# Optimization experiments

Measured on AMD Instinct MI355X. Metric: run time of the kernel, lower is better.

## Reference

```python
import jax, jax.numpy as jnp
import numpy as np

MAXDISP = 48
NUM_GROUPS = 40
CONCAT_CH = 12
BN_EPS = 1e-5


def conv3d(x, w):
    # x: [B,C,D,H,W], w: [O,I,3,3,3], stride 1, pad 1
    return jax.lax.conv_general_dilated(
        x, w, window_strides=(1, 1, 1), padding=[(1, 1), (1, 1), (1, 1)],
        dimension_numbers=('NCDHW', 'OIDHW', 'NCDHW'))


def bn_relu(x, gamma, beta, mean, var):
    # inference-style BatchNorm3d followed by ReLU
    inv = gamma * jax.lax.rsqrt(var + BN_EPS)
    sh = (1, -1, 1, 1, 1)
    return jax.nn.relu(x * inv.reshape(sh) + (beta - mean * inv).reshape(sh))


def build_volume(lg, rg, lc, rc):
    # Fused gwc + concat volume: for disparity d, valid region is columns [d:].
    # Columns [:d] are zero (matches the torch new_zeros + sliced writes).
    B, Cg, H, W = lg.shape
    cpg = Cg // NUM_GROUPS
    slices = []
    for d in range(MAXDISP):  # fixed structural loop over disparities
        if d == 0:
            l, r, lcc, rcc = lg, rg, lc, rc
        else:
            l = lg[:, :, :, d:]
            r = rg[:, :, :, :W - d]
            lcc = lc[:, :, :, d:]
            rcc = rc[:, :, :, :W - d]
        corr = (l * r).reshape(B, NUM_GROUPS, cpg, H, W - d).mean(axis=2)
        s = jnp.concatenate([corr, lcc, rcc], axis=1)  # [B, G+2Cc, H, W-d]
        if d > 0:
            s = jnp.pad(s, ((0, 0), (0, 0), (0, 0), (d, 0)))
        slices.append(s)
    return jnp.stack(slices, axis=2)  # [B, G+2Cc, D, H, W]


def setup_inputs() -> dict:
    key = jax.random.key(0)
    ks = jax.random.split(key, 10)
    B, H, W = 4, 64, 128
    Cin = NUM_GROUPS + 2 * CONCAT_CH  # 64
    f32 = jnp.float32
    return {
        'left_gwc': jax.random.normal(ks[0], (B, 320, H, W), f32),
        'right_gwc': jax.random.normal(ks[1], (B, 320, H, W), f32),
        'left_concat': jax.random.normal(ks[2], (B, CONCAT_CH, H, W), f32),
        'right_concat': jax.random.normal(ks[3], (B, CONCAT_CH, H, W), f32),
        'w1': jax.random.normal(ks[4], (32, Cin, 3, 3, 3), f32) * 0.05,
        'g1': jnp.ones((32,), f32),
        'b1': jnp.zeros((32,), f32),
        'm1': jnp.zeros((32,), f32),
        'v1': jnp.ones((32,), f32),
        'w2': jax.random.normal(ks[5], (32, 32, 3, 3, 3), f32) * 0.05,
        'g2': jnp.ones((32,), f32),
        'b2': jnp.zeros((32,), f32),
        'm2': jnp.zeros((32,), f32),
        'v2': jnp.ones((32,), f32),
    }


def reference(left_gwc, right_gwc, left_concat, right_concat,
              w1, g1, b1, m1, v1, w2, g2, b2, m2, v2):
    vol = build_volume(left_gwc, right_gwc, left_concat, right_concat)
    x = bn_relu(conv3d(vol, w1), g1, b1, m1, v1)
    x = bn_relu(conv3d(x, w2), g2, b2, m2, v2)
    return x  # [B, 32, D, H, W]
```

## Files before the change

kernel.cpp:

```cpp
#include <hip/hip_runtime.h>
#include <cstdint>
#include <cstddef>

typedef unsigned short u16;
typedef __bf16 bf16x8 __attribute__((ext_vector_type(8)));
typedef float f32x4 __attribute__((ext_vector_type(4)));

#define MAXDISP 48
#define HH 64
#define WW 128

__device__ __forceinline__ float bf2f(unsigned int x) {
    union { unsigned int i; float f; } c; c.i = x << 16; return c.f;
}
__device__ __forceinline__ float bf2f_hi(unsigned int x) {
    union { unsigned int i; float f; } c; c.i = x & 0xffff0000u; return c.f;
}
__device__ __forceinline__ u16 f2bf(float f) {
    union { float f; unsigned int i; } c; c.f = f;
    unsigned int x = c.i;
    return (u16)((x + 0x7fffu + ((x >> 16) & 1u)) >> 16);
}

__global__ __launch_bounds__(256) void wfrag_kernel(
    const float* __restrict__ w, const float* __restrict__ gam,
    const float* __restrict__ bet, const float* __restrict__ mea,
    const float* __restrict__ var,
    u16* __restrict__ dst, float* __restrict__ bias, int CIN, int KC)
{
    int idx = blockIdx.x * 256 + threadIdx.x;
    int n = 9 * 2 * KC * 512;
    if (idx < n) {
        int j    = idx & 7;
        int lane = (idx >> 3) & 63;
        int t2   = idx >> 9;
        int kc   = t2 % KC;
        int t3   = t2 / KC;
        int nt   = t3 & 1;
        int tap  = t3 >> 1;
        int co   = nt * 16 + (lane & 15);
        int qq   = lane >> 4;
        int kw, c;
        if (CIN == 64) { kw = kc >> 1; c = (kc & 1) * 32 + qq * 8 + j; }
        else           { kw = kc;      c = qq * 8 + j; }
        int kd = tap / 3, kh = tap % 3;
        float inv = gam[co] * rsqrtf(var[co] + 1e-5f);
        dst[idx] = f2bf(w[((size_t)co * CIN + c) * 27 + kd * 9 + kh * 3 + kw] * inv);
    }
    if (blockIdx.x == 0 && threadIdx.x < 32) {
        int co = threadIdx.x;
        float inv = gam[co] * rsqrtf(var[co] + 1e-5f);
        bias[co] = bet[co] - mea[co] * inv;
    }
}

#define RS 334
__global__ __launch_bounds__(256) void vol_build_kernel(
    const float* __restrict__ lg, const float* __restrict__ rg,
    const float* __restrict__ lc, const float* __restrict__ rc,
    u16* __restrict__ vol, int b0)
{
    __shared__ u16 r_s[128 * RS];
    __shared__ u16 o_s[4 * 128 * 68];

    int bi  = blockIdx.x;
    int h   = bi & 63;
    int dh  = (bi >> 6) & 1;
    int bl  = bi >> 7;
    int b   = b0 + bl;
    int tid = threadIdx.x;
    int w    = tid & 127;
    int part = tid >> 7;

    for (int idx = tid; idx < 320 * 32; idx += 256) {
        int c = idx >> 5, w4 = (idx & 31) << 2;
        const float4 v = *(const float4*)(rg + (((size_t)b * 320 + c) * 64 + h) * 128 + w4);
        r_s[(w4 + 0) * RS + c] = f2bf(v.x);
        r_s[(w4 + 1) * RS + c] = f2bf(v.y);
        r_s[(w4 + 2) * RS + c] = f2bf(v.z);
        r_s[(w4 + 3) * RS + c] = f2bf(v.w);
    }
    for (int idx = tid; idx < 12 * 32; idx += 256) {
        int c = idx >> 5, w4 = (idx & 31) << 2;
        const float4 v = *(const float4*)(rc + (((size_t)b * 12 + c) * 64 + h) * 128 + w4);
        r_s[(w4 + 0) * RS + 320 + c] = f2bf(v.x);
        r_s[(w4 + 1) * RS + 320 + c] = f2bf(v.y);
        r_s[(w4 + 2) * RS + 320 + c] = f2bf(v.z);
        r_s[(w4 + 3) * RS + 320 + c] = f2bf(v.w);
    }
    u16 lcv[12];
    if (part == 0) {
#pragma unroll
        for (int k = 0; k < 12; k++)
            lcv[k] = f2bf(lc[(((size_t)b * 12 + k) * 64 + h) * 128 + w]);
    }
    __syncthreads();

    int d0 = dh * 24;
    for (int dc = 0; dc < 24; dc += 4) {
        for (int gb = 0; gb < 5; gb++) {
            int g0 = part * 20 + gb * 4;
            float lv[4][8];
#pragma unroll
            for (int gg = 0; gg < 4; gg++)
#pragma unroll
                for (int j = 0; j < 8; j++)
                    lv[gg][j] = lg[(((size_t)b * 320 + (g0 + gg) * 8 + j) * 64 + h) * 128 + w];
#pragma unroll
            for (int dl = 0; dl < 4; dl++) {
                int d = d0 + dc + dl;
                union { u16 us[4]; uint2 u2; } pk;
                pk.us[0] = pk.us[1] = pk.us[2] = pk.us[3] = 0;
                if (w >= d) {
#pragma unroll
                    for (int gg = 0; gg < 4; gg++) {
                        float s = 0.f;
                        int base = (w - d) * RS + (g0 + gg) * 8;
#pragma unroll
                        for (int jj = 0; jj < 4; jj++) {
                            unsigned int uu = *(const unsigned int*)&r_s[base + jj * 2];
                            s += lv[gg][jj * 2]     * bf2f(uu & 0xffffu);
                            s += lv[gg][jj * 2 + 1] * bf2f_hi(uu);
                        }
                        pk.us[gg] = f2bf(s * 0.125f);
                    }
                }
                *(uint2*)&o_s[(dl * 128 + w) * 68 + g0] = pk.u2;
            }
        }
#pragma unroll
        for (int dl = 0; dl < 4; dl++) {
            int d = d0 + dc + dl;
            union { u16 us[12]; uint2 u2[3]; } z;
            if (part == 0) {
#pragma unroll
                for (int k = 0; k < 12; k++) z.us[k] = (w >= d) ? lcv[k] : (u16)0;
                u16* dst = &o_s[(dl * 128 + w) * 68 + 40];
                *(uint2*)(dst + 0) = z.u2[0];
                *(uint2*)(dst + 4) = z.u2[1];
                *(uint2*)(dst + 8) = z.u2[2];
            } else {
                if (w >= d) {
                    int base = (w - d) * RS + 320;
#pragma unroll
                    for (int k = 0; k < 12; k++) z.us[k] = r_s[base + k];
                } else {
#pragma unroll
                    for (int k = 0; k < 12; k++) z.us[k] = 0;
                }
                u16* dst = &o_s[(dl * 128 + w) * 68 + 52];
                *(uint2*)(dst + 0) = z.u2[0];
                *(uint2*)(dst + 4) = z.u2[1];
                *(uint2*)(dst + 8) = z.u2[2];
            }
        }
        __syncthreads();
#pragma unroll
        for (int i = 0; i < 16; i++) {
            int idx = i * 256 + tid;
            int dl  = idx >> 10;
            int rem = idx & 1023;
            int ww  = rem >> 3, cg = rem & 7;
            const u16* sp = &o_s[(dl * 128 + ww) * 68 + cg * 8];
            uint2 lo = *(const uint2*)sp;
            uint2 hi = *(const uint2*)(sp + 4);
            uint4 ov = { lo.x, lo.y, hi.x, hi.y };
            int d = d0 + dc + dl;
            *(uint4*)(vol + ((((size_t)bl * 48 + d) * 64 + h) * 128 + ww) * 64 + cg * 8) = ov;
        }
        __syncthreads();
    }
}

__global__ __launch_bounds__(256) void conv1_mfma_kernel(
    const u16* __restrict__ vol, const u16* __restrict__ wf,
    const float* __restrict__ bias, u16* __restrict__ x1)
{
    __shared__ u16 a_s[1170 * 8];

    int bi = blockIdx.x;
    int h  = bi & 63;
    int t1 = bi >> 6;
    int d  = t1 % 48;
    int bl = t1 / 48;
    int tid  = threadIdx.x;
    int lane = tid & 63, wid = tid >> 6;
    int lm = lane & 15, q = lane >> 4;

    f32x4 acc[2][2];
#pragma unroll
    for (int i = 0; i < 2; i++)
#pragma unroll
        for (int j = 0; j < 2; j++) acc[i][j] = { 0.f, 0.f, 0.f, 0.f };

    for (int kd = 0; kd < 3; kd++) {
        int dd = d + kd - 1;
        if (dd < 0 || dd >= 48) continue;
        for (int kh = 0; kh < 3; kh++) {
            int hh = h + kh - 1;
            if (hh < 0 || hh >= 64) continue;
            int tap = kd * 3 + kh;

            __syncthreads();
            const u16* src = vol + (((size_t)bl * 48 + dd) * 64 + hh) * 8192;
#pragma unroll
            for (int i = 0; i < 4; i++) {
                int idx = i * 256 + tid;
                int wp = (idx >> 3) + 1, cg = idx & 7;
                uint4 v = *(const uint4*)(src + idx * 8);
                *(uint4*)&a_s[(wp * 9 + cg) * 8] = v;
            }
            if (tid < 16) {
                uint4 z = { 0, 0, 0, 0 };
                int wp = (tid >> 3) ? 129 : 0;
                *(uint4*)&a_s[(wp * 9 + (tid & 7)) * 8] = z;
            }
            __syncthreads();

            bf16x8 bfr[2][6];
#pragma unroll
            for (int nt = 0; nt < 2; nt++)
#pragma unroll
                for (int kc = 0; kc < 6; kc++)
                    bfr[nt][kc] = *(const bf16x8*)(wf + (((size_t)tap * 2 + nt) * 6 + kc) * 512 + lane * 8);

#pragma unroll
            for (int kc = 0; kc < 6; kc++) {
                int kw = kc >> 1;
                int cg = (kc & 1) * 4 + q;
#pragma unroll
                for (int mt = 0; mt < 2; mt++) {
                    int wp = (wid * 2 + mt) * 16 + lm + kw;
                    bf16x8 afr = *(const bf16x8*)&a_s[(wp * 9 + cg) * 8];
                    acc[mt][0] = __builtin_amdgcn_mfma_f32_16x16x32_bf16(afr, bfr[0][kc], acc[mt][0], 0, 0, 0);
                    acc[mt][1] = __builtin_amdgcn_mfma_f32_16x16x32_bf16(afr, bfr[1][kc], acc[mt][1], 0, 0, 0);
                }
            }
        }
    }

    u16* xb = x1 + (((size_t)bl * 48 + d) * 64 + h) * 4096;
#pragma unroll
    for (int mt = 0; mt < 2; mt++)
#pragma unroll
        for (int nt = 0; nt < 2; nt++) {
            int co = nt * 16 + lm;
            float bs = bias[co];
#pragma unroll
            for (int r = 0; r < 4; r++) {
                int w = (wid * 2 + mt) * 16 + q * 4 + r;
                xb[w * 32 + co] = f2bf(fmaxf(acc[mt][nt][r] + bs, 0.f));
            }
        }
}

__global__ __launch_bounds__(256) void conv2_mfma_kernel(
    const u16* __restrict__ x1, const u16* __restrict__ wf,
    const float* __restrict__ bias, float* __restrict__ out, int b0)
{
    __shared__ u16 a_s[650 * 8];

    int bi = blockIdx.x;
    int h  = bi & 63;
    int t1 = bi >> 6;
    int d  = t1 % 48;
    int bl = t1 / 48;
    int tid  = threadIdx.x;
    int lane = tid & 63, wid = tid >> 6;
    int lm = lane & 15, q = lane >> 4;

    f32x4 acc[2][2];
#pragma unroll
    for (int i = 0; i < 2; i++)
#pragma unroll
        for (int j = 0; j < 2; j++) acc[i][j] = { 0.f, 0.f, 0.f, 0.f };

    for (int kd = 0; kd < 3; kd++) {
        int dd = d + kd - 1;
        if (dd < 0 || dd >= 48) continue;
        for (int kh = 0; kh < 3; kh++) {
            int hh = h + kh - 1;
            if (hh < 0 || hh >= 64) continue;
            int tap = kd * 3 + kh;

            __syncthreads();
            const u16* src = x1 + (((size_t)bl * 48 + dd) * 64 + hh) * 4096;
#pragma unroll
            for (int i = 0; i < 2; i++) {
                int idx = i * 256 + tid;
                int wp = (idx >> 2) + 1, cg = idx & 3;
                uint4 v = *(const uint4*)(src + idx * 8);
                *(uint4*)&a_s[(wp * 5 + cg) * 8] = v;
            }
            if (tid < 8) {
                uint4 z = { 0, 0, 0, 0 };
                int wp = (tid >> 2) ? 129 : 0;
                *(uint4*)&a_s[(wp * 5 + (tid & 3)) * 8] = z;
            }
            __syncthreads();

            bf16x8 bfr[2][3];
#pragma unroll
            for (int nt = 0; nt < 2; nt++)
#pragma unroll
                for (int kc = 0; kc < 3; kc++)
                    bfr[nt][kc] = *(const bf16x8*)(wf + (((size_t)tap * 2 + nt) * 3 + kc) * 512 + lane * 8);

#pragma unroll
            for (int kc = 0; kc < 3; kc++) {
                int kw = kc;
#pragma unroll
                for (int mt = 0; mt < 2; mt++) {
                    int wp = (wid * 2 + mt) * 16 + lm + kw;
                    bf16x8 afr = *(const bf16x8*)&a_s[(wp * 5 + q) * 8];
                    acc[mt][0] = __builtin_amdgcn_mfma_f32_16x16x32_bf16(afr, bfr[0][kc], acc[mt][0], 0, 0, 0);
                    acc[mt][1] = __builtin_amdgcn_mfma_f32_16x16x32_bf16(afr, bfr[1][kc], acc[mt][1], 0, 0, 0);
                }
            }
        }
    }

#pragma unroll
    for (int mt = 0; mt < 2; mt++)
#pragma unroll
        for (int nt = 0; nt < 2; nt++) {
            int co = nt * 16 + lm;
            float bs = bias[co];
            float4 o;
            o.x = fmaxf(acc[mt][nt][0] + bs, 0.f);
            o.y = fmaxf(acc[mt][nt][1] + bs, 0.f);
            o.z = fmaxf(acc[mt][nt][2] + bs, 0.f);
            o.w = fmaxf(acc[mt][nt][3] + bs, 0.f);
            int wbase = (wid * 2 + mt) * 16 + q * 4;
            *(float4*)(out + ((((size_t)(b0 + bl) * 32 + co) * 48 + d) * 64 + h) * 128 + wbase) = o;
        }
}

extern "C" void kernel_launch(void* const* d_in, const int* in_sizes, int n_in,
                              void* d_out, int out_size, void* d_ws, size_t ws_size,
                              hipStream_t stream)
{
    const float* lg = (const float*)d_in[0];
    const float* rg = (const float*)d_in[1];
    const float* lc = (const float*)d_in[2];
    const float* rc = (const float*)d_in[3];
    const float* w1 = (const float*)d_in[4];
    const float* g1 = (const float*)d_in[5];
    const float* b1 = (const float*)d_in[6];
    const float* m1 = (const float*)d_in[7];
    const float* v1 = (const float*)d_in[8];
    const float* w2 = (const float*)d_in[9];
    const float* g2 = (const float*)d_in[10];
    const float* b2 = (const float*)d_in[11];
    const float* m2 = (const float*)d_in[12];
    const float* v2 = (const float*)d_in[13];
    (void)in_sizes; (void)n_in; (void)out_size; (void)ws_size;

    char* ws = (char*)d_ws;
    u16*   wf1   = (u16*)ws;
    u16*   wf2   = (u16*)(ws + 110592);
    float* bias1 = (float*)(ws + 165888);
    float* bias2 = (float*)(ws + 166016);
    u16*   x1    = (u16*)(ws + 166144);

    wfrag_kernel<<<216, 256, 0, stream>>>(w1, g1, b1, m1, v1, wf1, bias1, 64, 6);
    wfrag_kernel<<<108, 256, 0, stream>>>(w2, g2, b2, m2, v2, wf2, bias2, 32, 3);

    for (int r = 0; r < 2; r++) {
        u16* vol = (u16*)d_out + (size_t)r * 50331648;
        vol_build_kernel<<<256, 256, 0, stream>>>(lg, rg, lc, rc, vol, 2 * r);
        conv1_mfma_kernel<<<6144, 256, 0, stream>>>(vol, wf1, bias1, x1);
        conv2_mfma_kernel<<<6144, 256, 0, stream>>>(x1, wf2, bias2, (float*)d_out, 2 * r);
    }
}
```

Before: 802.5 us.

## Tile conv kernels over 2x2 output depth-height blocks to reuse input rows

Each conv block now computes a 2x2 tile of output (depth, height) rows. It loads the 4 overlapping input height rows per depth slice into shared memory once and reuses them across all four outputs, instead of reloading 9 input rows per output row. conv1 splits the 64 input channels into two 32-channel chunks to fit shared memory. The volume-build kernel is split into 4 depth quarters to double its grid. This raises accumulator register pressure (launch_bounds 256,3) and cuts the conv grids by four.

After: 979.1 us. 22.0% more time.

```diff
diff --git a/kernel.cpp b/kernel.cpp
--- a/kernel.cpp
+++ b/kernel.cpp
@@ -65,8 +65,8 @@
 
     int bi  = blockIdx.x;
     int h   = bi & 63;
-    int dh  = (bi >> 6) & 1;
-    int bl  = bi >> 7;
+    int dq  = (bi >> 6) & 3;
+    int bl  = bi >> 8;
     int b   = b0 + bl;
     int tid = threadIdx.x;
     int w    = tid & 127;
@@ -96,8 +96,8 @@
     }
     __syncthreads();
 
-    int d0 = dh * 24;
-    for (int dc = 0; dc < 24; dc += 4) {
+    int d0 = dq * 12;
+    for (int dc = 0; dc < 12; dc += 4) {
         for (int gb = 0; gb < 5; gb++) {
             int g0 = part * 20 + gb * 4;
             float lv[4][8];
@@ -172,168 +172,212 @@
     }
 }
 
-__global__ __launch_bounds__(256) void conv1_mfma_kernel(
+__global__ __launch_bounds__(256, 3) void conv1_mfma_kernel(
     const u16* __restrict__ vol, const u16* __restrict__ wf,
     const float* __restrict__ bias, u16* __restrict__ x1)
 {
-    __shared__ u16 a_s[1170 * 8];
+    __shared__ u16 a_s[4][5200];
 
     int bi = blockIdx.x;
-    int h  = bi & 63;
-    int t1 = bi >> 6;
-    int d  = t1 % 48;
-    int bl = t1 / 48;
+    int ht = bi & 31;
+    int dt = (bi >> 5) % 24;
+    int bl = bi / 768;
+    int h0 = ht * 2, d0 = dt * 2;
     int tid  = threadIdx.x;
     int lane = tid & 63, wid = tid >> 6;
     int lm = lane & 15, q = lane >> 4;
 
-    f32x4 acc[2][2];
-#pragma unroll
-    for (int i = 0; i < 2; i++)
-#pragma unroll
-        for (int j = 0; j < 2; j++) acc[i][j] = { 0.f, 0.f, 0.f, 0.f };
-
-    for (int kd = 0; kd < 3; kd++) {
-        int dd = d + kd - 1;
+    f32x4 acc[2][2][2][2];
+#pragma unroll
+    for (int a = 0; a < 2; a++)
+#pragma unroll
+        for (int o = 0; o < 2; o++)
+#pragma unroll
+            for (int m = 0; m < 2; m++)
+#pragma unroll
+                for (int n = 0; n < 2; n++) acc[a][o][m][n] = { 0.f, 0.f, 0.f, 0.f };
+
+#pragma unroll 1
+    for (int dr = 0; dr < 4; dr++) {
+        int dd = d0 - 1 + dr;
         if (dd < 0 || dd >= 48) continue;
-        for (int kh = 0; kh < 3; kh++) {
-            int hh = h + kh - 1;
-            if (hh < 0 || hh >= 64) continue;
-            int tap = kd * 3 + kh;
-
+        const u16* srcbase = vol + ((size_t)bl * 48 + dd) * 64 * 8192;
+        int od0v = (dr <= 2), od1v = (dr >= 1);
+
+#pragma unroll 1
+        for (int ch = 0; ch < 2; ch++) {
             __syncthreads();
-            const u16* src = vol + (((size_t)bl * 48 + dd) * 64 + hh) * 8192;
-#pragma unroll
-            for (int i = 0; i < 4; i++) {
+#pragma unroll
+            for (int i = 0; i < 8; i++) {
                 int idx = i * 256 + tid;
-                int wp = (idx >> 3) + 1, cg = idx & 7;
-                uint4 v = *(const uint4*)(src + idx * 8);
-                *(uint4*)&a_s[(wp * 9 + cg) * 8] = v;
-            }
-            if (tid < 16) {
+                int r = idx >> 9, rem = idx & 511;
+                int w = rem >> 2, cg = rem & 3;
+                int hh = h0 - 1 + r;
+                uint4 v = { 0, 0, 0, 0 };
+                if (hh >= 0 && hh < 64)
+                    v = *(const uint4*)(srcbase + (size_t)hh * 8192 + w * 64 + ch * 32 + cg * 8);
+                *(uint4*)&a_s[r][((w + 1) * 5 + cg) * 8] = v;
+            }
+            if (tid < 32) {
                 uint4 z = { 0, 0, 0, 0 };
-                int wp = (tid >> 3) ? 129 : 0;
-                *(uint4*)&a_s[(wp * 9 + (tid & 7)) * 8] = z;
+                int r = tid >> 3, side = (tid >> 2) & 1, cg = tid & 3;
+                *(uint4*)&a_s[r][((side ? 129 : 0) * 5 + cg) * 8] = z;
             }
             __syncthreads();
 
-            bf16x8 bfr[2][6];
-#pragma unroll
-            for (int nt = 0; nt < 2; nt++)
-#pragma unroll
-                for (int kc = 0; kc < 6; kc++)
-                    bfr[nt][kc] = *(const bf16x8*)(wf + (((size_t)tap * 2 + nt) * 6 + kc) * 512 + lane * 8);
-
-#pragma unroll
-            for (int kc = 0; kc < 6; kc++) {
-                int kw = kc >> 1;
-                int cg = (kc & 1) * 4 + q;
-#pragma unroll
-                for (int mt = 0; mt < 2; mt++) {
-                    int wp = (wid * 2 + mt) * 16 + lm + kw;
-                    bf16x8 afr = *(const bf16x8*)&a_s[(wp * 9 + cg) * 8];
-                    acc[mt][0] = __builtin_amdgcn_mfma_f32_16x16x32_bf16(afr, bfr[0][kc], acc[mt][0], 0, 0, 0);
-                    acc[mt][1] = __builtin_amdgcn_mfma_f32_16x16x32_bf16(afr, bfr[1][kc], acc[mt][1], 0, 0, 0);
-                }
-            }
-        }
-    }
-
-    u16* xb = x1 + (((size_t)bl * 48 + d) * 64 + h) * 4096;
-#pragma unroll
-    for (int mt = 0; mt < 2; mt++)
-#pragma unroll
-        for (int nt = 0; nt < 2; nt++) {
-            int co = nt * 16 + lm;
-            float bs = bias[co];
 #pragma unroll
             for (int r = 0; r < 4; r++) {
-                int w = (wid * 2 + mt) * 16 + q * 4 + r;
-                xb[w * 32 + co] = f2bf(fmaxf(acc[mt][nt][r] + bs, 0.f));
-            }
-        }
-}
-
-__global__ __launch_bounds__(256) void conv2_mfma_kernel(
+#pragma unroll
+                for (int kw = 0; kw < 3; kw++) {
+                    int kc = kw * 2 + ch;
+                    bf16x8 afr[2];
+#pragma unroll
+                    for (int mt = 0; mt < 2; mt++)
+                        afr[mt] = *(const bf16x8*)&a_s[r][((((wid * 2 + mt) * 16 + lm + kw) * 5) + q) * 8];
+#pragma unroll
+                    for (int od = 0; od < 2; od++) {
+                        if (od == 0 ? !od0v : !od1v) continue;
+                        int kd = dr - od;
+#pragma unroll
+                        for (int oh = 0; oh < 2; oh++) {
+                            if (oh == 0 ? (r > 2) : (r < 1)) continue;
+                            int kh = r - oh;
+                            int tap = kd * 3 + kh;
+                            const u16* wp0 = wf + ((size_t)(tap * 2) * 6 + kc) * 512 + lane * 8;
+                            bf16x8 b0 = *(const bf16x8*)wp0;
+                            bf16x8 b1 = *(const bf16x8*)(wp0 + 6 * 512);
+#pragma unroll
+                            for (int mt = 0; mt < 2; mt++) {
+                                acc[od][oh][mt][0] = __builtin_amdgcn_mfma_f32_16x16x32_bf16(afr[mt], b0, acc[od][oh][mt][0], 0, 0, 0);
+                                acc[od][oh][mt][1] = __builtin_amdgcn_mfma_f32_16x16x32_bf16(afr[mt], b1, acc[od][oh][mt][1], 0, 0, 0);
+                            }
+                        }
+                    }
+                }
+            }
+        }
+    }
+
+#pragma unroll
+    for (int od = 0; od < 2; od++)
+#pragma unroll
+        for (int oh = 0; oh < 2; oh++) {
+            u16* xb = x1 + (((size_t)bl * 48 + d0 + od) * 64 + h0 + oh) * 4096;
+#pragma unroll
+            for (int mt = 0; mt < 2; mt++)
+#pragma unroll
+                for (int nt = 0; nt < 2; nt++) {
+                    int co = nt * 16 + lm;
+                    float bs = bias[co];
+#pragma unroll
+                    for (int rr = 0; rr < 4; rr++) {
+                        int w = (wid * 2 + mt) * 16 + q * 4 + rr;
+                        xb[w * 32 + co] = f2bf(fmaxf(acc[od][oh][mt][nt][rr] + bs, 0.f));
+                    }
+                }
+        }
+}
+
+__global__ __launch_bounds__(256, 3) void conv2_mfma_kernel(
     const u16* __restrict__ x1, const u16* __restrict__ wf,
     const float* __restrict__ bias, float* __restrict__ out, int b0)
 {
-    __shared__ u16 a_s[650 * 8];
+    __shared__ u16 a_s[4][5200];
 
     int bi = blockIdx.x;
-    int h  = bi & 63;
-    int t1 = bi >> 6;
-    int d  = t1 % 48;
-    int bl = t1 / 48;
+    int ht = bi & 31;
+    int dt = (bi >> 5) % 24;
+    int bl = bi / 768;
+    int h0 = ht * 2, d0 = dt * 2;
     int tid  = threadIdx.x;
     int lane = tid & 63, wid = tid >> 6;
     int lm = lane & 15, q = lane >> 4;
 
-    f32x4 acc[2][2];
-#pragma unroll
-    for (int i = 0; i < 2; i++)
-#pragma unroll
-        for (int j = 0; j < 2; j++) acc[i][j] = { 0.f, 0.f, 0.f, 0.f };
-
-    for (int kd = 0; kd < 3; kd++) {
-        int dd = d + kd - 1;
+    f32x4 acc[2][2][2][2];
+#pragma unroll
+    for (int a = 0; a < 2; a++)
+#pragma unroll
+        for (int o = 0; o < 2; o++)
+#pragma unroll
+            for (int m = 0; m < 2; m++)
+#pragma unroll
+                for (int n = 0; n < 2; n++) acc[a][o][m][n] = { 0.f, 0.f, 0.f, 0.f };
+
+#pragma unroll 1
+    for (int dr = 0; dr < 4; dr++) {
+        int dd = d0 - 1 + dr;
         if (dd < 0 || dd >= 48) continue;
-        for (int kh = 0; kh < 3; kh++) {
-            int hh = h + kh - 1;
-            if (hh < 0 || hh >= 64) continue;
-            int tap = kd * 3 + kh;
-
-            __syncthreads();
-            const u16* src = x1 + (((size_t)bl * 48 + dd) * 64 + hh) * 4096;
-#pragma unroll
-            for (int i = 0; i < 2; i++) {
-                int idx = i * 256 + tid;
-                int wp = (idx >> 2) + 1, cg = idx & 3;
-                uint4 v = *(const uint4*)(src + idx * 8);
-                *(uint4*)&a_s[(wp * 5 + cg) * 8] = v;
-            }
-            if (tid < 8) {
-                uint4 z = { 0, 0, 0, 0 };
-                int wp = (tid >> 2) ? 129 : 0;
-                *(uint4*)&a_s[(wp * 5 + (tid & 3)) * 8] = z;
-            }
-            __syncthreads();
-
-            bf16x8 bfr[2][3];
-#pragma unroll
-            for (int nt = 0; nt < 2; nt++)
-#pragma unroll
-                for (int kc = 0; kc < 3; kc++)
-                    bfr[nt][kc] = *(const bf16x8*)(wf + (((size_t)tap * 2 + nt) * 3 + kc) * 512 + lane * 8);
-
-#pragma unroll
-            for (int kc = 0; kc < 3; kc++) {
-                int kw = kc;
-#pragma unroll
-                for (int mt = 0; mt < 2; mt++) {
-                    int wp = (wid * 2 + mt) * 16 + lm + kw;
-                    bf16x8 afr = *(const bf16x8*)&a_s[(wp * 5 + q) * 8];
-                    acc[mt][0] = __builtin_amdgcn_mfma_f32_16x16x32_bf16(afr, bfr[0][kc], acc[mt][0], 0, 0, 0);
-                    acc[mt][1] = __builtin_amdgcn_mfma_f32_16x16x32_bf16(afr, bfr[1][kc], acc[mt][1], 0, 0, 0);
-                }
-            }
-        }
-    }
-
-#pragma unroll
-    for (int mt = 0; mt < 2; mt++)
-#pragma unroll
-        for (int nt = 0; nt < 2; nt++) {
-            int co = nt * 16 + lm;
-            float bs = bias[co];
-            float4 o;
-            o.x = fmaxf(acc[mt][nt][0] + bs, 0.f);
-            o.y = fmaxf(acc[mt][nt][1] + bs, 0.f);
-            o.z = fmaxf(acc[mt][nt][2] + bs, 0.f);
-            o.w = fmaxf(acc[mt][nt][3] + bs, 0.f);
-            int wbase = (wid * 2 + mt) * 16 + q * 4;
-            *(float4*)(out + ((((size_t)(b0 + bl) * 32 + co) * 48 + d) * 64 + h) * 128 + wbase) = o;
-        }
+        const u16* srcbase = x1 + ((size_t)bl * 48 + dd) * 64 * 4096;
+        int od0v = (dr <= 2), od1v = (dr >= 1);
+
+        __syncthreads();
+#pragma unroll
+        for (int i = 0; i < 8; i++) {
+            int idx = i * 256 + tid;
+            int r = idx >> 9, rem = idx & 511;
+            int w = rem >> 2, cg = rem & 3;
+            int hh = h0 - 1 + r;
+            uint4 v = { 0, 0, 0, 0 };
+            if (hh >= 0 && hh < 64)
+                v = *(const uint4*)(srcbase + (size_t)hh * 4096 + w * 32 + cg * 8);
+            *(uint4*)&a_s[r][((w + 1) * 5 + cg) * 8] = v;
+        }
+        if (tid < 32) {
+            uint4 z = { 0, 0, 0, 0 };
+            int r = tid >> 3, side = (tid >> 2) & 1, cg = tid & 3;
+            *(uint4*)&a_s[r][((side ? 129 : 0) * 5 + cg) * 8] = z;
+        }
+        __syncthreads();
+
+#pragma unroll
+        for (int r = 0; r < 4; r++) {
+#pragma unroll
+            for (int kw = 0; kw < 3; kw++) {
+                bf16x8 afr[2];
+#pragma unroll
+                for (int mt = 0; mt < 2; mt++)
+                    afr[mt] = *(const bf16x8*)&a_s[r][((((wid * 2 + mt) * 16 + lm + kw) * 5) + q) * 8];
+#pragma unroll
+                for (int od = 0; od < 2; od++) {
+                    if (od == 0 ? !od0v : !od1v) continue;
+                    int kd = dr - od;
+#pragma unroll
+                    for (int oh = 0; oh < 2; oh++) {
+                        if (oh == 0 ? (r > 2) : (r < 1)) continue;
+                        int kh = r - oh;
+                        int tap = kd * 3 + kh;
+                        const u16* wp0 = wf + ((size_t)(tap * 2) * 3 + kw) * 512 + lane * 8;
+                        bf16x8 b0 = *(const bf16x8*)wp0;
+                        bf16x8 b1 = *(const bf16x8*)(wp0 + 3 * 512);
+#pragma unroll
+                        for (int mt = 0; mt < 2; mt++) {
+                            acc[od][oh][mt][0] = __builtin_amdgcn_mfma_f32_16x16x32_bf16(afr[mt], b0, acc[od][oh][mt][0], 0, 0, 0);
+                            acc[od][oh][mt][1] = __builtin_amdgcn_mfma_f32_16x16x32_bf16(afr[mt], b1, acc[od][oh][mt][1], 0, 0, 0);
+                        }
+                    }
+                }
+            }
+        }
+    }
+
+#pragma unroll
+    for (int od = 0; od < 2; od++)
+#pragma unroll
+        for (int oh = 0; oh < 2; oh++)
+#pragma unroll
+            for (int mt = 0; mt < 2; mt++)
+#pragma unroll
+                for (int nt = 0; nt < 2; nt++) {
+                    int co = nt * 16 + lm;
+                    float bs = bias[co];
+                    float4 o;
+                    o.x = fmaxf(acc[od][oh][mt][nt][0] + bs, 0.f);
+                    o.y = fmaxf(acc[od][oh][mt][nt][1] + bs, 0.f);
+                    o.z = fmaxf(acc[od][oh][mt][nt][2] + bs, 0.f);
+                    o.w = fmaxf(acc[od][oh][mt][nt][3] + bs, 0.f);
+                    int wbase = (wid * 2 + mt) * 16 + q * 4;
+                    *(float4*)(out + ((((size_t)(b0 + bl) * 32 + co) * 48 + d0 + od) * 64 + h0 + oh) * 128 + wbase) = o;
+                }
 }
 
 extern "C" void kernel_launch(void* const* d_in, const int* in_sizes, int n_in,
@@ -368,8 +412,8 @@
 
     for (int r = 0; r < 2; r++) {
         u16* vol = (u16*)d_out + (size_t)r * 50331648;
-        vol_build_kernel<<<256, 256, 0, stream>>>(lg, rg, lc, rc, vol, 2 * r);
-        conv1_mfma_kernel<<<6144, 256, 0, stream>>>(vol, wf1, bias1, x1);
-        conv2_mfma_kernel<<<6144, 256, 0, stream>>>(x1, wf2, bias2, (float*)d_out, 2 * r);
-    }
-}
+        vol_build_kernel<<<512, 256, 0, stream>>>(lg, rg, lc, rc, vol, 2 * r);
+        conv1_mfma_kernel<<<1536, 256, 0, stream>>>(vol, wf1, bias1, x1);
+        conv2_mfma_kernel<<<1536, 256, 0, stream>>>(x1, wf2, bias2, (float*)d_out, 2 * r);
+    }
+}
```

## Double-buffer conv input rows with register prefetch and split volume build finer

Applied to the files above, without the earlier changes.

The conv1 and conv2 kernels now list their valid taps up front and use double-buffered shared memory. Each loop iteration prefetches the next tap's input row into registers while the current tap's MFMAs run, which removes one barrier per tap and hides global load latency. Launch bounds now request minimum occupancy. The volume build splits disparities into quarters instead of halves, launching twice as many blocks for better CU coverage. In exchange, each volume block reloads and converts the full right-feature row, doubling that redundant work, and conv shared memory and register use go up.

New measurement: 1.546 ms. 92.6% more time.

```diff
diff --git a/kernel.cpp b/kernel.cpp
--- a/kernel.cpp
+++ b/kernel.cpp
@@ -65,8 +65,8 @@
 
     int bi  = blockIdx.x;
     int h   = bi & 63;
-    int dh  = (bi >> 6) & 1;
-    int bl  = bi >> 7;
+    int dq  = (bi >> 6) & 3;
+    int bl  = bi >> 8;
     int b   = b0 + bl;
     int tid = threadIdx.x;
     int w    = tid & 127;
@@ -96,8 +96,8 @@
     }
     __syncthreads();
 
-    int d0 = dh * 24;
-    for (int dc = 0; dc < 24; dc += 4) {
+    int d0 = dq * 12;
+    for (int dc = 0; dc < 12; dc += 4) {
         for (int gb = 0; gb < 5; gb++) {
             int g0 = part * 20 + gb * 4;
             float lv[4][8];
@@ -172,11 +172,11 @@
     }
 }
 
-__global__ __launch_bounds__(256) void conv1_mfma_kernel(
+__global__ __launch_bounds__(256, 3) void conv1_mfma_kernel(
     const u16* __restrict__ vol, const u16* __restrict__ wf,
     const float* __restrict__ bias, u16* __restrict__ x1)
 {
-    __shared__ u16 a_s[1170 * 8];
+    __shared__ u16 a_s[2][1170 * 8];
 
     int bi = blockIdx.x;
     int h  = bi & 63;
@@ -187,54 +187,74 @@
     int lane = tid & 63, wid = tid >> 6;
     int lm = lane & 15, q = lane >> 4;
 
-    f32x4 acc[2][2];
-#pragma unroll
-    for (int i = 0; i < 2; i++)
-#pragma unroll
-        for (int j = 0; j < 2; j++) acc[i][j] = { 0.f, 0.f, 0.f, 0.f };
-
+    if (tid < 32) {
+        uint4 z = { 0, 0, 0, 0 };
+        int bsel = tid >> 4, side = (tid >> 3) & 1, cg = tid & 7;
+        *(uint4*)&a_s[bsel][((side ? 129 : 0) * 9 + cg) * 8] = z;
+    }
+
+    int trow[9], ttap[9], ntap = 0;
     for (int kd = 0; kd < 3; kd++) {
         int dd = d + kd - 1;
         if (dd < 0 || dd >= 48) continue;
         for (int kh = 0; kh < 3; kh++) {
             int hh = h + kh - 1;
             if (hh < 0 || hh >= 64) continue;
-            int tap = kd * 3 + kh;
-
-            __syncthreads();
-            const u16* src = vol + (((size_t)bl * 48 + dd) * 64 + hh) * 8192;
-#pragma unroll
-            for (int i = 0; i < 4; i++) {
-                int idx = i * 256 + tid;
-                int wp = (idx >> 3) + 1, cg = idx & 7;
-                uint4 v = *(const uint4*)(src + idx * 8);
-                *(uint4*)&a_s[(wp * 9 + cg) * 8] = v;
-            }
-            if (tid < 16) {
-                uint4 z = { 0, 0, 0, 0 };
-                int wp = (tid >> 3) ? 129 : 0;
-                *(uint4*)&a_s[(wp * 9 + (tid & 7)) * 8] = z;
-            }
-            __syncthreads();
-
-            bf16x8 bfr[2][6];
-#pragma unroll
-            for (int nt = 0; nt < 2; nt++)
-#pragma unroll
-                for (int kc = 0; kc < 6; kc++)
-                    bfr[nt][kc] = *(const bf16x8*)(wf + (((size_t)tap * 2 + nt) * 6 + kc) * 512 + lane * 8);
-
-#pragma unroll
-            for (int kc = 0; kc < 6; kc++) {
-                int kw = kc >> 1;
-                int cg = (kc & 1) * 4 + q;
-#pragma unroll
-                for (int mt = 0; mt < 2; mt++) {
-                    int wp = (wid * 2 + mt) * 16 + lm + kw;
-                    bf16x8 afr = *(const bf16x8*)&a_s[(wp * 9 + cg) * 8];
-                    acc[mt][0] = __builtin_amdgcn_mfma_f32_16x16x32_bf16(afr, bfr[0][kc], acc[mt][0], 0, 0, 0);
-                    acc[mt][1] = __builtin_amdgcn_mfma_f32_16x16x32_bf16(afr, bfr[1][kc], acc[mt][1], 0, 0, 0);
-                }
+            trow[ntap] = dd * 64 + hh;
+            ttap[ntap] = kd * 3 + kh;
+            ntap++;
+        }
+    }
+    const u16* vbase = vol + (size_t)bl * 48 * 64 * 8192;
+
+    f32x4 acc[2][2];
+#pragma unroll
+    for (int i = 0; i < 2; i++)
+#pragma unroll
+        for (int j = 0; j < 2; j++) acc[i][j] = { 0.f, 0.f, 0.f, 0.f };
+
+    uint4 pf[4];
+    {
+        const u16* src = vbase + (size_t)trow[0] * 8192;
+#pragma unroll
+        for (int i = 0; i < 4; i++) pf[i] = *(const uint4*)(src + (i * 256 + tid) * 8);
+    }
+
+#pragma unroll 1
+    for (int t = 0; t < ntap; t++) {
+        u16* buf = a_s[t & 1];
+#pragma unroll
+        for (int i = 0; i < 4; i++) {
+            int idx = i * 256 + tid;
+            int wp = (idx >> 3) + 1, cg = idx & 7;
+            *(uint4*)&buf[(wp * 9 + cg) * 8] = pf[i];
+        }
+        __syncthreads();
+
+        int tap = ttap[t];
+        bf16x8 bfr[2][6];
+#pragma unroll
+        for (int nt = 0; nt < 2; nt++)
+#pragma unroll
+            for (int kc = 0; kc < 6; kc++)
+                bfr[nt][kc] = *(const bf16x8*)(wf + (((size_t)tap * 2 + nt) * 6 + kc) * 512 + lane * 8);
+
+        if (t + 1 < ntap) {
+            const u16* src = vbase + (size_t)trow[t + 1] * 8192;
+#pragma unroll
+            for (int i = 0; i < 4; i++) pf[i] = *(const uint4*)(src + (i * 256 + tid) * 8);
+        }
+
+#pragma unroll
+        for (int kc = 0; kc < 6; kc++) {
+            int kw = kc >> 1;
+            int cg = (kc & 1) * 4 + q;
+#pragma unroll
+            for (int mt = 0; mt < 2; mt++) {
+                int wp = (wid * 2 + mt) * 16 + lm + kw;
+                bf16x8 afr = *(const bf16x8*)&buf[(wp * 9 + cg) * 8];
+                acc[mt][0] = __builtin_amdgcn_mfma_f32_16x16x32_bf16(afr, bfr[0][kc], acc[mt][0], 0, 0, 0);
+                acc[mt][1] = __builtin_amdgcn_mfma_f32_16x16x32_bf16(afr, bfr[1][kc], acc[mt][1], 0, 0, 0);
             }
         }
     }
@@ -254,11 +274,11 @@
         }
 }
 
-__global__ __launch_bounds__(256) void conv2_mfma_kernel(
+__global__ __launch_bounds__(256, 4) void conv2_mfma_kernel(
     const u16* __restrict__ x1, const u16* __restrict__ wf,
     const float* __restrict__ bias, float* __restrict__ out, int b0)
 {
-    __shared__ u16 a_s[650 * 8];
+    __shared__ u16 a_s[2][650 * 8];
 
     int bi = blockIdx.x;
     int h  = bi & 63;
@@ -269,53 +289,73 @@
     int lane = tid & 63, wid = tid >> 6;
     int lm = lane & 15, q = lane >> 4;
 
-    f32x4 acc[2][2];
-#pragma unroll
-    for (int i = 0; i < 2; i++)
-#pragma unroll
-        for (int j = 0; j < 2; j++) acc[i][j] = { 0.f, 0.f, 0.f, 0.f };
-
+    if (tid < 16) {
+        uint4 z = { 0, 0, 0, 0 };
+        int bsel = tid >> 3, side = (tid >> 2) & 1, cg = tid & 3;
+        *(uint4*)&a_s[bsel][((side ? 129 : 0) * 5 + cg) * 8] = z;
+    }
+
+    int trow[9], ttap[9], ntap = 0;
     for (int kd = 0; kd < 3; kd++) {
         int dd = d + kd - 1;
         if (dd < 0 || dd >= 48) continue;
         for (int kh = 0; kh < 3; kh++) {
             int hh = h + kh - 1;
             if (hh < 0 || hh >= 64) continue;
-            int tap = kd * 3 + kh;
-
-            __syncthreads();
-            const u16* src = x1 + (((size_t)bl * 48 + dd) * 64 + hh) * 4096;
-#pragma unroll
-            for (int i = 0; i < 2; i++) {
-                int idx = i * 256 + tid;
-                int wp = (idx >> 2) + 1, cg = idx & 3;
-                uint4 v = *(const uint4*)(src + idx * 8);
-                *(uint4*)&a_s[(wp * 5 + cg) * 8] = v;
-            }
-            if (tid < 8) {
-                uint4 z = { 0, 0, 0, 0 };
-                int wp = (tid >> 2) ? 129 : 0;
-                *(uint4*)&a_s[(wp * 5 + (tid & 3)) * 8] = z;
-            }
-            __syncthreads();
-
-            bf16x8 bfr[2][3];
-#pragma unroll
-            for (int nt = 0; nt < 2; nt++)
-#pragma unroll
-                for (int kc = 0; kc < 3; kc++)
-                    bfr[nt][kc] = *(const bf16x8*)(wf + (((size_t)tap * 2 + nt) * 3 + kc) * 512 + lane * 8);
-
-#pragma unroll
-            for (int kc = 0; kc < 3; kc++) {
-                int kw = kc;
-#pragma unroll
-                for (int mt = 0; mt < 2; mt++) {
-                    int wp = (wid * 2 + mt) * 16 + lm + kw;
-                    bf16x8 afr = *(const bf16x8*)&a_s[(wp * 5 + q) * 8];
-                    acc[mt][0] = __builtin_amdgcn_mfma_f32_16x16x32_bf16(afr, bfr[0][kc], acc[mt][0], 0, 0, 0);
-                    acc[mt][1] = __builtin_amdgcn_mfma_f32_16x16x32_bf16(afr, bfr[1][kc], acc[mt][1], 0, 0, 0);
-                }
+            trow[ntap] = dd * 64 + hh;
+            ttap[ntap] = kd * 3 + kh;
+            ntap++;
+        }
+    }
+    const u16* xbase = x1 + (size_t)bl * 48 * 64 * 4096;
+
+    f32x4 acc[2][2];
+#pragma unroll
+    for (int i = 0; i < 2; i++)
+#pragma unroll
+        for (int j = 0; j < 2; j++) acc[i][j] = { 0.f, 0.f, 0.f, 0.f };
+
+    uint4 pf[2];
+    {
+        const u16* src = xbase + (size_t)trow[0] * 4096;
+#pragma unroll
+        for (int i = 0; i < 2; i++) pf[i] = *(const uint4*)(src + (i * 256 + tid) * 8);
+    }
+
+#pragma unroll 1
+    for (int t = 0; t < ntap; t++) {
+        u16* buf = a_s[t & 1];
+#pragma unroll
+        for (int i = 0; i < 2; i++) {
+            int idx = i * 256 + tid;
+            int wp = (idx >> 2) + 1, cg = idx & 3;
+            *(uint4*)&buf[(wp * 5 + cg) * 8] = pf[i];
+        }
+        __syncthreads();
+
+        int tap = ttap[t];
+        bf16x8 bfr[2][3];
+#pragma unroll
+        for (int nt = 0; nt < 2; nt++)
+#pragma unroll
+            for (int kc = 0; kc < 3; kc++)
+                bfr[nt][kc] = *(const bf16x8*)(wf + (((size_t)tap * 2 + nt) * 3 + kc) * 512 + lane * 8);
+
+        if (t + 1 < ntap) {
+            const u16* src = xbase + (size_t)trow[t + 1] * 4096;
+#pragma unroll
+            for (int i = 0; i < 2; i++) pf[i] = *(const uint4*)(src + (i * 256 + tid) * 8);
+        }
+
+#pragma unroll
+        for (int kc = 0; kc < 3; kc++) {
+            int kw = kc;
+#pragma unroll
+            for (int mt = 0; mt < 2; mt++) {
+                int wp = (wid * 2 + mt) * 16 + lm + kw;
+                bf16x8 afr = *(const bf16x8*)&buf[(wp * 5 + q) * 8];
+                acc[mt][0] = __builtin_amdgcn_mfma_f32_16x16x32_bf16(afr, bfr[0][kc], acc[mt][0], 0, 0, 0);
+                acc[mt][1] = __builtin_amdgcn_mfma_f32_16x16x32_bf16(afr, bfr[1][kc], acc[mt][1], 0, 0, 0);
             }
         }
     }
@@ -368,7 +408,7 @@
 
     for (int r = 0; r < 2; r++) {
         u16* vol = (u16*)d_out + (size_t)r * 50331648;
-        vol_build_kernel<<<256, 256, 0, stream>>>(lg, rg, lc, rc, vol, 2 * r);
+        vol_build_kernel<<<512, 256, 0, stream>>>(lg, rg, lc, rc, vol, 2 * r);
         conv1_mfma_kernel<<<6144, 256, 0, stream>>>(vol, wf1, bias1, x1);
         conv2_mfma_kernel<<<6144, 256, 0, stream>>>(x1, wf2, bias2, (float*)d_out, 2 * r);
     }
```
